# Performance work log

Hardware: AMD Instinct MI355X
Metric: run time of the kernel (lower is better)

The kernel has to match this reference:

```python
import jax, jax.numpy as jnp
import numpy as np

GROUP_SIZES = [2048, 4096, 8192, 16384]
TOP_K = 64
L1_COEFF = 1e-3
AUX_PENALTY = 1e-2
N_BATCHES_TO_DEAD = 20
AUX_K_MULT = 16


def setup_inputs() -> dict:
    D = 1024
    S = sum(GROUP_SIZES)  # 30720
    B = 2048
    key = jax.random.key(0)
    k1, k2, k3 = jax.random.split(key, 3)
    x = jax.random.normal(k1, (B, D), dtype=jnp.float32)
    # kaiming_uniform-like init for W_enc [D, S]
    bound = np.sqrt(6.0 / D)
    W_enc = jax.random.uniform(k2, (D, S), jnp.float32, -bound, bound)
    # W_dec = W_enc.T row-normalized (as in __init__)
    W_dec = W_enc.T
    W_dec = W_dec / jnp.linalg.norm(W_dec, axis=-1, keepdims=True)
    b_dec = jnp.zeros((D,), jnp.float32)
    b_enc = jnp.zeros((S,), jnp.float32)
    num_batches_not_active = jax.random.randint(k3, (S,), 0, 40, dtype=jnp.int32)
    return dict(x=x, b_dec=b_dec, b_enc=b_enc, W_enc=W_enc, W_dec=W_dec,
                num_batches_not_active=num_batches_not_active)


def reference(x, b_dec, b_enc, W_enc, W_dec, num_batches_not_active):
    B, D = x.shape
    S = W_enc.shape[1]
    # encoder
    acts = jax.nn.relu((x - b_dec) @ W_enc + b_enc)  # [B, S]
    # global (batch-level) top-k over flattened activations + scatter back
    k = TOP_K * B
    flat = acts.reshape(-1)
    vals, idx = jax.lax.top_k(flat, k)
    acts_topk = jnp.zeros_like(flat).at[idx].set(vals).reshape(B, S)
    # hierarchical group-wise decode with per-group L2 losses
    bounds = np.concatenate([[0], np.cumsum(GROUP_SIZES)]).astype(int)
    recon = jnp.broadcast_to(b_dec, (B, D))
    l2_losses = []
    for i in range(len(GROUP_SIZES)):
        s, e = int(bounds[i]), int(bounds[i + 1])
        recon = recon + acts_topk[:, s:e] @ W_dec[s:e, :]
        l2_losses.append(jnp.mean((recon - x) ** 2))
    mean_l2_loss = jnp.mean(jnp.stack(l2_losses))
    l1_loss = L1_COEFF * jnp.mean(jnp.sum(jnp.abs(acts_topk), axis=-1))
    # auxiliary dead-feature loss
    dead = num_batches_not_active >= N_BATCHES_TO_DEAD  # [S] bool
    residual = jax.lax.stop_gradient(x - recon)
    k_aux = TOP_K * AUX_K_MULT * B  # assumes num_dead * B >= k_aux (holds here)
    masked = jnp.where(dead[None, :], acts, -jnp.inf)
    min_top_k_val = jax.lax.top_k(masked.reshape(-1), k_aux)[0][-1]
    min_top_k_val = jnp.where(jnp.isfinite(min_top_k_val), min_top_k_val, 0.0)
    acts_aux = jax.nn.relu(acts - min_top_k_val) * dead[None, :].astype(acts.dtype)
    recon_aux = acts_aux @ W_dec  # dead-only contribution (others zeroed)
    aux_loss = AUX_PENALTY * jnp.mean((recon_aux - residual) ** 2)
    aux_loss = jnp.where(jnp.any(dead), aux_loss, 0.0)
    total_loss = mean_l2_loss + l1_loss + aux_loss
    l0_norm = jnp.mean(jnp.sum((acts_topk > 0).astype(jnp.float32), axis=-1))
    return total_loss, mean_l2_loss, l1_loss, aux_loss, l0_norm, acts_topk, recon
```

## Files before the change

### kernel.cpp

```cpp
#include <hip/hip_runtime.h>

#define NB 2048
#define ND 1024
#define NS 30720
#define K_MAIN 131072LL
#define K_AUX  2097152LL
#define BAND_CAP 16384
#define SEL_CAP  8192
#define CANDA_CAP 65536
#define EPS_BAND 1e-3f
#define KSPLIT 4

#define OFF_SCAL 0
#define OFF_ACC  256
#define OFF_H1M  512
#define OFF_H1A  16896
#define OFF_H2M  33280
#define OFF_H2A  49664
#define OFF_ZERO_END 66048
#define OFF_DEAD 66048
#define OFF_SEL_IDX 98304
#define OFF_SEL_BITS 131072
#define OFF_BANDI 163840
#define OFF_BANDV 229376
#define OFF_CAB  360448
#define OFF_RAUX 1048576ULL
#define OFF_AH   (OFF_RAUX + (unsigned long long)KSPLIT * NB * ND * 4)
#define OFF_AL   (OFF_AH + 2048ULL*1024*2)
#define OFF_WHT  (OFF_AL + 2048ULL*1024*2)
#define OFF_WLT  (OFF_WHT + 30720ULL*1024*2)
#define WS_NEED_ENC (OFF_WLT + 30720ULL*1024*2)
#define OFF_AXB  OFF_AH
#define OFF_WDT  (OFF_AXB + 2048ULL*30720*2)
#define WS_NEED_AUX (OFF_WDT + 1024ULL*30720*2)

#define S_NDEAD 0
#define S_B1M 1
#define S_REM1M 2
#define S_B1A 3
#define S_REM1A 4
#define S_T24M 5
#define S_BLO 6
#define S_BHI 7
#define S_T24A 8
#define S_JA 9
#define S_NHI 10
#define S_BANDC 11
#define S_CCA 12
#define S_SELCNT 13
#define S_L0 14
#define S_MINBITS 15

#define A_L2_0 0
#define A_L1 4
#define A_AUX 5

typedef __attribute__((ext_vector_type(8))) short bf16x8;
typedef __attribute__((ext_vector_type(4))) float f32x4;

__device__ __forceinline__ float blk_reduce(float v, float* sred) {
    int t = threadIdx.x;
    #pragma unroll
    for (int o = 32; o > 0; o >>= 1) v += __shfl_down(v, o, 64);
    __syncthreads();
    if ((t & 63) == 0) sred[t >> 6] = v;
    __syncthreads();
    return sred[0] + sred[1] + sred[2] + sred[3];
}

__device__ __forceinline__ unsigned short f2bf(float f) {
    unsigned u = __float_as_uint(f);
    unsigned r = (u + 0x7FFFu + ((u >> 16) & 1u)) >> 16;
    return (unsigned short)r;
}
__device__ __forceinline__ float bf2f(unsigned short h) {
    return __uint_as_float(((unsigned)h) << 16);
}

#define GLD16(gp, lp) __builtin_amdgcn_global_load_lds( \
    (const __attribute__((address_space(1))) unsigned int*)(gp), \
    (__attribute__((address_space(3))) unsigned int*)(lp), 16, 0, 0)

__global__ void k_init(int* w) {
    int n = OFF_ZERO_END / 4;
    for (int i = blockIdx.x * blockDim.x + threadIdx.x; i < n; i += gridDim.x * blockDim.x)
        w[i] = 0;
}

__global__ void k_dead(const int* __restrict__ nbna, unsigned char* __restrict__ dead, int* scal) {
    int stride = gridDim.x * blockDim.x;
    int cnt = 0;
    for (int i = blockIdx.x * blockDim.x + threadIdx.x; i < NS; i += stride) {
        bool d = nbna[i] >= 20;
        dead[i] = d ? 1 : 0;
        cnt += d ? 1 : 0;
    }
    #pragma unroll
    for (int o = 32; o > 0; o >>= 1) cnt += __shfl_down(cnt, o, 64);
    if ((threadIdx.x & 63) == 0 && cnt) atomicAdd(&scal[S_NDEAD], cnt);
}

__global__ void k_prep_a(const float* __restrict__ x, const float* __restrict__ b_dec,
                         unsigned short* __restrict__ Ahg, unsigned short* __restrict__ Alg) {
    int stride = gridDim.x * blockDim.x;
    for (int i = blockIdx.x * blockDim.x + threadIdx.x; i < NB * ND; i += stride) {
        float v = x[i] - b_dec[i & (ND - 1)];
        unsigned short h = f2bf(v);
        unsigned short l = f2bf(v - bf2f(h));
        Ahg[i] = h; Alg[i] = l;
    }
}

__global__ __launch_bounds__(256) void k_prep_w(const float* __restrict__ W,
        unsigned short* __restrict__ WhT, unsigned short* __restrict__ WlT) {
    __shared__ float tile[32][33];
    int n0 = blockIdx.x * 32, k0 = blockIdx.y * 32;
    int t = threadIdx.x;
    int c = t & 31, r = t >> 5;
    #pragma unroll
    for (int it = 0; it < 4; it++)
        tile[r + it * 8][c] = W[(size_t)(k0 + r + it * 8) * NS + n0 + c];
    __syncthreads();
    int kl = t & 31, nl = t >> 5;
    #pragma unroll
    for (int it = 0; it < 4; it++) {
        float v = tile[kl][nl + it * 8];
        unsigned short h = f2bf(v);
        unsigned short l = f2bf(v - bf2f(h));
        size_t o = (size_t)(n0 + nl + it * 8) * ND + k0 + kl;
        WhT[o] = h; WlT[o] = l;
    }
}

#define ENC_STAGE(bufoff, p, gptr, r, ktn) GLD16((gptr) + (size_t)(r) * 128 * ND + (size_t)(ktn) * 32, \
    smem + (bufoff) + (p) * 8192 + (r) * 4096 + ldsw)

#define ENC_RD_AH(boff) { _Pragma("unroll") \
    for (int i = 0; i < 8; i++) ah[i] = *(const bf16x8*)&smem[(boff) + (arb + i * 16) * 32 + cph8]; }
#define ENC_RD_BH(boff) { _Pragma("unroll") \
    for (int j = 0; j < 4; j++) bh[j] = *(const bf16x8*)&smem[(boff) + 2 * 8192 + (brb + j * 16) * 32 + cph8]; }
#define ENC_RD_BL(boff) { _Pragma("unroll") \
    for (int j = 0; j < 4; j++) bl[j] = *(const bf16x8*)&smem[(boff) + 3 * 8192 + (brb + j * 16) * 32 + cph8]; }
#define ENC_RD_AL(boff) { _Pragma("unroll") \
    for (int i = 0; i < 8; i++) al[i] = *(const bf16x8*)&smem[(boff) + 8192 + (arb + i * 16) * 32 + cph8]; }

#define ENC_MFMA(AF, BF) { \
    asm volatile("s_waitcnt lgkmcnt(0)" ::: "memory"); \
    __builtin_amdgcn_sched_barrier(0); \
    __builtin_amdgcn_s_setprio(1); \
    _Pragma("unroll") for (int i = 0; i < 8; i++) \
        _Pragma("unroll") for (int j = 0; j < 4; j++) \
            acc[i][j] = __builtin_amdgcn_mfma_f32_16x16x32_bf16(AF[i], BF[j], acc[i][j], 0, 0, 0); \
    __builtin_amdgcn_s_setprio(0); }

__global__ __launch_bounds__(512, 2) void k_enc_mfma(
        const unsigned short* __restrict__ Ahg, const unsigned short* __restrict__ Alg,
        const unsigned short* __restrict__ WhT, const unsigned short* __restrict__ WlT,
        const float* __restrict__ b_enc, float* __restrict__ acts) {
    __shared__ unsigned short smem[65536];
    const int t = threadIdx.x;
    const int lane = t & 63, w = t >> 6;
    const int wm = w >> 2, wn = w & 3;
    const int flat = blockIdx.x;
    const int wg = (flat & 7) * 120 + (flat >> 3);
    const int n0 = (wg >> 3) * 256;
    const int m0 = (wg & 7) * 256;
    const int ln15 = lane & 15, q = lane >> 4;
    const int cph8 = ((q ^ ((lane >> 1) & 3)) << 3);

    const int srow = w * 16 + (lane >> 2);
    const int sq8 = (((lane & 3) ^ ((lane >> 3) & 3)) << 3);
    const unsigned short* gA  = Ahg + (size_t)(m0 + srow) * ND + sq8;
    const unsigned short* gAl = Alg + (size_t)(m0 + srow) * ND + sq8;
    const unsigned short* gB  = WhT + (size_t)(n0 + srow) * ND + sq8;
    const unsigned short* gBl = WlT + (size_t)(n0 + srow) * ND + sq8;
    const int ldsw = w * 512;

    f32x4 acc[8][4];
    #pragma unroll
    for (int i = 0; i < 8; i++)
        #pragma unroll
        for (int j = 0; j < 4; j++) acc[i][j] = (f32x4){0.f, 0.f, 0.f, 0.f};

    const int arb = wm * 128 + ln15;
    const int brb = wn * 64 + ln15;

    ENC_STAGE(0, 0, gA, 0, 0);  ENC_STAGE(0, 0, gA, 1, 0);
    ENC_STAGE(0, 2, gB, 0, 0);  ENC_STAGE(0, 2, gB, 1, 0);
    ENC_STAGE(0, 3, gBl, 0, 0); ENC_STAGE(0, 3, gBl, 1, 0);
    ENC_STAGE(0, 1, gAl, 0, 0); ENC_STAGE(0, 1, gAl, 1, 0);

    for (int kt = 0; kt < 31; ++kt) {
        const int cboff = (kt & 1) * 32768;
        const int nboff = cboff ^ 32768;
        const int kn = kt + 1;
        bf16x8 ah[8], bh[4], bl[4], al[8];

        ENC_STAGE(nboff, 0, gA, 0, kn);  ENC_STAGE(nboff, 0, gA, 1, kn);
        ENC_STAGE(nboff, 2, gB, 0, kn);  ENC_STAGE(nboff, 2, gB, 1, kn);
        asm volatile("s_waitcnt vmcnt(8)" ::: "memory");
        __builtin_amdgcn_s_barrier();
        ENC_RD_AH(cboff) ENC_RD_BH(cboff)
        ENC_MFMA(ah, bh)

        ENC_STAGE(nboff, 3, gBl, 0, kn); ENC_STAGE(nboff, 3, gBl, 1, kn);
        ENC_STAGE(nboff, 1, gAl, 0, kn); ENC_STAGE(nboff, 1, gAl, 1, kn);
        asm volatile("s_waitcnt vmcnt(8)" ::: "memory");
        __builtin_amdgcn_s_barrier();
        ENC_RD_BL(cboff)
        ENC_MFMA(ah, bl)

        ENC_RD_AL(cboff)
        ENC_MFMA(al, bh)
    }

    {
        const int cboff = 32768;
        bf16x8 ah[8], bh[4], bl[4], al[8];
        asm volatile("s_waitcnt vmcnt(4)" ::: "memory");
        __builtin_amdgcn_s_barrier();
        ENC_RD_AH(cboff) ENC_RD_BH(cboff)
        ENC_MFMA(ah, bh)
        asm volatile("s_waitcnt vmcnt(0)" ::: "memory");
        __builtin_amdgcn_s_barrier();
        ENC_RD_BL(cboff)
        ENC_MFMA(ah, bl)
        ENC_RD_AL(cboff)
        ENC_MFMA(al, bh)
    }

    #pragma unroll
    for (int j = 0; j < 4; j++) {
        int n = n0 + wn * 64 + j * 16 + ln15;
        float be = b_enc[n];
        #pragma unroll
        for (int i = 0; i < 8; i++) {
            int mrow = m0 + wm * 128 + i * 16 + q * 4;
            #pragma unroll
            for (int rg = 0; rg < 4; rg++)
                acts[(size_t)(mrow + rg) * NS + n] = fmaxf(acc[i][j][rg] + be, 0.f);
        }
    }
}

#define GBM 128
#define GBN 128
#define GBK 8
__global__ __launch_bounds__(256) void k_enc_gemm(const float* __restrict__ x,
        const float* __restrict__ b_dec, const float* __restrict__ b_enc,
        const float* __restrict__ W, float* __restrict__ acts) {
    __shared__ float As[GBK][GBM];
    __shared__ float Bs[GBK][GBN];
    const int t = threadIdx.x;
    const int tx = t & 15, ty = t >> 4;
    const int m0 = blockIdx.y * GBM, n0 = blockIdx.x * GBN;
    const int am = t >> 1, ak = (t & 1) * 4;
    const int bk = t >> 5, bnq = (t & 31) * 4;
    float acc[8][8];
    #pragma unroll
    for (int i = 0; i < 8; i++)
        #pragma unroll
        for (int j = 0; j < 8; j++) acc[i][j] = 0.f;
    for (int k0 = 0; k0 < ND; k0 += GBK) {
        float4 av = *(const float4*)(x + (size_t)(m0 + am) * ND + k0 + ak);
        float4 bd = *(const float4*)(b_dec + k0 + ak);
        As[ak + 0][am] = av.x - bd.x;
        As[ak + 1][am] = av.y - bd.y;
        As[ak + 2][am] = av.z - bd.z;
        As[ak + 3][am] = av.w - bd.w;
        *(float4*)&Bs[bk][bnq] = *(const float4*)(W + (size_t)(k0 + bk) * NS + n0 + bnq);
        __syncthreads();
        #pragma unroll
        for (int kk = 0; kk < GBK; kk++) {
            float a[8], b[8];
            *(float4*)&a[0] = *(const float4*)&As[kk][ty * 4];
            *(float4*)&a[4] = *(const float4*)&As[kk][64 + ty * 4];
            *(float4*)&b[0] = *(const float4*)&Bs[kk][tx * 4];
            *(float4*)&b[4] = *(const float4*)&Bs[kk][64 + tx * 4];
            #pragma unroll
            for (int i = 0; i < 8; i++)
                #pragma unroll
                for (int j = 0; j < 8; j++)
                    acc[i][j] = fmaf(a[i], b[j], acc[i][j]);
        }
        __syncthreads();
    }
    float be[8];
    #pragma unroll
    for (int j = 0; j < 4; j++) {
        be[j]     = b_enc[n0 + tx * 4 + j];
        be[4 + j] = b_enc[n0 + 64 + tx * 4 + j];
    }
    #pragma unroll
    for (int i = 0; i < 8; i++) {
        int row = m0 + ((i < 4) ? (ty * 4 + i) : (64 + ty * 4 + i - 4));
        float* orow = acts + (size_t)row * NS + n0;
        #pragma unroll
        for (int j = 0; j < 4; j++) {
            orow[tx * 4 + j]      = fmaxf(acc[i][j] + be[j], 0.f);
            orow[64 + tx * 4 + j] = fmaxf(acc[i][4 + j] + be[4 + j], 0.f);
        }
    }
}

__global__ __launch_bounds__(256) void k_hist1(const float* __restrict__ acts,
        const unsigned char* __restrict__ dead, int* h1m, int* h1a) {
    __shared__ int hm[4096], ha[4096];
    int t = threadIdx.x;
    for (int i = t; i < 4096; i += 256) { hm[i] = 0; ha[i] = 0; }
    __syncthreads();
    for (int row = blockIdx.x; row < NB; row += gridDim.x) {
        const float* pr = acts + (size_t)row * NS;
        for (int c = t; c < NS; c += 256) {
            unsigned bits = __float_as_uint(pr[c]);
            bool isz = (bits == 0u);
            bool dd = dead[c] != 0;
            unsigned long long mz = __ballot(isz);
            unsigned long long mza = __ballot(isz && dd);
            if ((t & 63) == 0) {
                int nz = __popcll(mz);
                if (nz) atomicAdd(&hm[0], nz);
                int nza = __popcll(mza);
                if (nza) atomicAdd(&ha[0], nza);
            }
            if (!isz) {
                atomicAdd(&hm[bits >> 20], 1);
                if (dd) atomicAdd(&ha[bits >> 20], 1);
            }
        }
    }
    __syncthreads();
    for (int i = t; i < 4096; i += 256) {
        if (hm[i]) atomicAdd(&h1m[i], hm[i]);
        if (ha[i]) atomicAdd(&h1a[i], ha[i]);
    }
}

__global__ void k_scan(const int* __restrict__ hist, int* scal, int mode) {
    __shared__ long long csum[256];
    __shared__ long long totsh;
    int t = threadIdx.x;
    int base = t * 16;
    int h[16];
    long long loc = 0;
    #pragma unroll
    for (int i = 0; i < 16; i++) { h[i] = hist[base + i]; loc += h[i]; }
    csum[t] = loc;
    __syncthreads();
    if (t == 0) {
        long long run = 0;
        for (int c = 255; c >= 0; c--) { long long tmp = csum[c]; csum[c] = run; run += tmp; }
        totsh = run;
    }
    __syncthreads();
    long long k;
    if (mode == 0) k = K_MAIN;
    else if (mode == 1) k = K_AUX;
    else if (mode == 2) k = (long long)scal[S_REM1M];
    else {
        if (scal[S_B1A] < 0) { if (t == 0) { scal[S_T24A] = -1; scal[S_MINBITS] = 0; } return; }
        k = (long long)scal[S_REM1A];
    }
    if (mode == 1 && k > totsh) { if (t == 0) scal[S_B1A] = -1; return; }
    long long cum = csum[t];
    int fb = -1; long long rem = 0;
    for (int i = 15; i >= 0; i--) {
        long long ca = cum;
        cum += h[i];
        if (ca < k && k <= cum) { fb = base + i; rem = k - ca; }
    }
    if (fb >= 0) {
        if (mode == 0)      { scal[S_B1M] = fb; scal[S_REM1M] = (int)rem; }
        else if (mode == 1) { scal[S_B1A] = fb; scal[S_REM1A] = (int)rem; }
        else if (mode == 2) {
            int t24 = (scal[S_B1M] << 12) | fb;
            scal[S_T24M] = t24;
            float center = __uint_as_float((((unsigned)t24) << 8) | 128u);
            float lo = center - EPS_BAND;
            if (lo < 0.f) lo = 0.f;
            scal[S_BLO] = (int)__float_as_uint(lo);
            scal[S_BHI] = (int)__float_as_uint(center + EPS_BAND);
        }
        else { scal[S_T24A] = (scal[S_B1A] << 12) | fb; scal[S_JA] = (int)rem; }
    }
}

__global__ __launch_bounds__(256) void k_hist2(const float* __restrict__ acts,
        const unsigned char* __restrict__ dead, const int* scal, int* h2m, int* h2a) {
    int b1m = scal[S_B1M], b1a = scal[S_B1A];
    int row = blockIdx.x, t = threadIdx.x;
    const float* pr = acts + (size_t)row * NS;
    for (int c = t; c < NS; c += 256) {
        unsigned bits = __float_as_uint(pr[c]);
        int hi = (int)(bits >> 20);
        if (hi == b1m) atomicAdd(&h2m[(bits >> 8) & 0xFFF], 1);
        if (b1a >= 0 && hi == b1a && dead[c]) atomicAdd(&h2a[(bits >> 8) & 0xFFF], 1);
    }
}

__global__ __launch_bounds__(256) void k_collect(const float* __restrict__ acts,
        const unsigned char* __restrict__ dead, int* scal,
        int* bandi, unsigned* cab) {
    int row = blockIdx.x, t = threadIdx.x;
    unsigned blo = (unsigned)scal[S_BLO], bhi = (unsigned)scal[S_BHI];
    int t24a = scal[S_T24A];
    const float* pr = acts + (size_t)row * NS;
    int cnt = 0;
    for (int c = t; c < NS; c += 256) {
        unsigned bits = __float_as_uint(pr[c]);
        if (bits > bhi) cnt++;
        else if (bits >= blo) {
            int p = atomicAdd(&scal[S_BANDC], 1);
            if (p < BAND_CAP) bandi[p] = row * NS + c;
        }
        if (t24a >= 0 && (bits >> 8) == (unsigned)t24a && dead[c]) {
            int p = atomicAdd(&scal[S_CCA], 1);
            if (p < CANDA_CAP) cab[p] = bits;
        }
    }
    #pragma unroll
    for (int o = 32; o > 0; o >>= 1) cnt += __shfl_down(cnt, o, 64);
    __shared__ int s2[4];
    if ((t & 63) == 0) s2[t >> 6] = cnt;
    __syncthreads();
    if (t == 0) {
        int tot = s2[0] + s2[1] + s2[2] + s2[3];
        if (tot) atomicAdd(&scal[S_NHI], tot);
    }
}

__global__ __launch_bounds__(256) void k_resolve(const unsigned* __restrict__ cab, int* scal) {
    __shared__ int h[256];
    int t = threadIdx.x;
    h[t] = 0;
    __syncthreads();
    int t24a = scal[S_T24A];
    if (t24a < 0) { if (t == 0) scal[S_MINBITS] = 0; return; }
    int cnt = min(scal[S_CCA], CANDA_CAP);
    int ja = scal[S_JA];
    for (int e = t; e < cnt; e += 256) atomicAdd(&h[cab[e] & 0xFF], 1);
    __syncthreads();
    if (t == 0) {
        long long cum = 0; int L = 0;
        for (int b = 255; b >= 0; b--) {
            long long ca = cum; cum += h[b];
            if (ca < ja && ja <= cum) { L = b; break; }
        }
        scal[S_MINBITS] = (int)((((unsigned)t24a) << 8) | (unsigned)L);
    }
}

__global__ __launch_bounds__(256) void k_band_re(const float* __restrict__ x,
        const float* __restrict__ b_dec, const float* __restrict__ b_enc,
        const float* __restrict__ W, const int* scal,
        const int* __restrict__ bandi, double* __restrict__ bandv) {
    int n = min(scal[S_BANDC], BAND_CAP);
    int t = threadIdx.x;
    __shared__ double sd[4];
    for (int e = blockIdx.x; e < n; e += gridDim.x) {
        int idx = bandi[e];
        int r = idx / NS, c = idx - r * NS;
        double s = 0.0;
        #pragma unroll
        for (int j = 0; j < 4; j++) {
            int d = t + j * 256;
            s += ((double)x[(size_t)r * ND + d] - (double)b_dec[d]) * (double)W[(size_t)d * NS + c];
        }
        #pragma unroll
        for (int o = 32; o > 0; o >>= 1) s += __shfl_down(s, o, 64);
        if ((t & 63) == 0) sd[t >> 6] = s;
        __syncthreads();
        if (t == 0) {
            double v = sd[0] + sd[1] + sd[2] + sd[3] + (double)b_enc[c];
            bandv[e] = fmax(v, 0.0);
        }
        __syncthreads();
    }
}

__global__ __launch_bounds__(256) void k_band_sel(int* scal,
        const int* __restrict__ bandi, const double* __restrict__ bandv,
        int* sel_idx, unsigned* sel_bits) {
    int n = min(scal[S_BANDC], BAND_CAP);
    int need = (int)(K_MAIN - (long long)scal[S_NHI]);
    if (need < 0) need = 0;
    if (need > n) need = n;
    int t = threadIdx.x;
    for (int e = t; e < n; e += 256) {
        double v = bandv[e];
        int idx = bandi[e];
        int rank = 0;
        for (int j = 0; j < n; j++) {
            double vj = bandv[j];
            rank += (vj > v || (vj == v && bandi[j] < idx)) ? 1 : 0;
        }
        if (rank < need) {
            int p = atomicAdd(&scal[S_SELCNT], 1);
            if (p < SEL_CAP) { sel_idx[p] = idx; sel_bits[p] = __float_as_uint((float)v); }
        }
    }
}

__global__ __launch_bounds__(256) void k_decode(const float* __restrict__ acts,
        const float* __restrict__ x, const float* __restrict__ b_dec, const float* __restrict__ Wd,
        float* __restrict__ recon, const int* scal,
        const int* __restrict__ sel_idx, double* acc) {
    int row = blockIdx.x, t = threadIdx.x;
    unsigned blo = (unsigned)scal[S_BLO], bhi = (unsigned)scal[S_BHI];
    int selcnt = min(scal[S_SELCNT], SEL_CAP);
    __shared__ int lj[2048];
    __shared__ float lv[2048];
    __shared__ int lcnt;
    __shared__ float sred[4];
    const int d0 = t * 4;
    float4 r;
    r.x = b_dec[d0]; r.y = b_dec[d0 + 1]; r.z = b_dec[d0 + 2]; r.w = b_dec[d0 + 3];
    float4 xv = *(const float4*)(x + (size_t)row * ND + d0);
    const float* arow = acts + (size_t)row * NS;
    const int bnds[5] = {0, 2048, 6144, 14336, NS};
    for (int g = 0; g < 4; g++) {
        for (int c0 = bnds[g]; c0 < bnds[g + 1]; c0 += 2048) {
            __syncthreads();
            if (t == 0) lcnt = 0;
            __syncthreads();
            #pragma unroll
            for (int u = 0; u < 8; u++) {
                int c = c0 + u * 256 + t;
                float v = arow[c];
                unsigned bits = __float_as_uint(v);
                bool keep = bits > bhi;
                if (!keep && bits >= blo) {
                    int flat = row * NS + c;
                    for (int e = 0; e < selcnt; e++)
                        if (sel_idx[e] == flat) { keep = true; break; }
                }
                if (keep) { int p = atomicAdd(&lcnt, 1); lj[p] = c; lv[p] = v; }
            }
            __syncthreads();
            int n = lcnt;
            for (int e = 0; e < n; e++) {
                float a_ = lv[e];
                float4 w = *(const float4*)(Wd + (size_t)lj[e] * ND + d0);
                r.x = fmaf(a_, w.x, r.x);
                r.y = fmaf(a_, w.y, r.y);
                r.z = fmaf(a_, w.z, r.z);
                r.w = fmaf(a_, w.w, r.w);
            }
        }
        float dx = r.x - xv.x, dy = r.y - xv.y, dz = r.z - xv.z, dw = r.w - xv.w;
        float ss = dx * dx + dy * dy + dz * dz + dw * dw;
        float tot = blk_reduce(ss, sred);
        if (t == 0) atomicAdd(&acc[A_L2_0 + g], (double)tot);
    }
    float* orow = recon + (size_t)row * ND + d0;
    orow[0] = r.x; orow[1] = r.y; orow[2] = r.z; orow[3] = r.w;
}

__global__ __launch_bounds__(256) void k_aux_pack(const float* __restrict__ acts,
        const unsigned char* __restrict__ dead, const int* scal,
        unsigned short* __restrict__ axb) {
    int row = blockIdx.x, t = threadIdx.x;
    float minval = __uint_as_float((unsigned)scal[S_MINBITS]);
    const float* arow = acts + (size_t)row * NS;
    unsigned short* orow = axb + (size_t)row * NS;
    for (int c = t; c < NS; c += 256) {
        float v = arow[c];
        float o = (dead[c] && v > minval) ? (v - minval) : 0.f;
        orow[c] = f2bf(o);
    }
}

__global__ __launch_bounds__(256) void k_prep_wd(const float* __restrict__ Wd,
        unsigned short* __restrict__ WdT) {
    __shared__ float tile[32][33];
    int s0 = blockIdx.x * 32, d0 = blockIdx.y * 32;
    int t = threadIdx.x;
    int c = t & 31, r = t >> 5;
    #pragma unroll
    for (int it = 0; it < 4; it++)
        tile[r + it * 8][c] = Wd[(size_t)(s0 + r + it * 8) * ND + d0 + c];
    __syncthreads();
    int sl = t & 31, dl = t >> 5;
    #pragma unroll
    for (int it = 0; it < 4; it++)
        WdT[(size_t)(d0 + dl + it * 8) * NS + s0 + sl] = f2bf(tile[sl][dl + it * 8]);
}

__global__ __launch_bounds__(256) void k_aux_mfma(
        const unsigned short* __restrict__ axb, const unsigned short* __restrict__ WdT,
        float* __restrict__ raux) {
    __shared__ unsigned short As[128 * 32], Bs[128 * 32];
    const int t = threadIdx.x;
    const int lane = t & 63, w = t >> 6;
    const int wm = w >> 1, wn = w & 1;
    const int m0 = blockIdx.y * 128, n0 = blockIdx.x * 128;
    const int kbase = blockIdx.z * (NS / KSPLIT);
    const int ln15 = lane & 15, q = lane >> 4;

    f32x4 acc[4][4];
    #pragma unroll
    for (int i = 0; i < 4; i++)
        #pragma unroll
        for (int j = 0; j < 4; j++) acc[i][j] = (f32x4){0.f, 0.f, 0.f, 0.f};

    const unsigned short* gbase;
    unsigned short* lbase;
    if (w < 2) { gbase = axb + (size_t)(m0 + w * 64) * NS; lbase = As + w * 64 * 32; }
    else       { gbase = WdT + (size_t)(n0 + (w - 2) * 64) * NS; lbase = Bs + (w - 2) * 64 * 32; }
    const unsigned short* glane = gbase + (size_t)(lane >> 2) * NS + (lane & 3) * 8 + kbase;

    for (int k0 = 0; k0 < NS / KSPLIT; k0 += 32) {
        __syncthreads();
        #pragma unroll
        for (int ch = 0; ch < 4; ch++)
            GLD16(glane + (size_t)ch * 16 * NS + k0, lbase + ch * 512);
        __syncthreads();

        bf16x8 af[4];
        #pragma unroll
        for (int i = 0; i < 4; i++)
            af[i] = *(const bf16x8*)&As[(wm * 64 + i * 16 + ln15) * 32 + q * 8];
        #pragma unroll
        for (int j = 0; j < 4; j++) {
            bf16x8 bf = *(const bf16x8*)&Bs[(wn * 64 + j * 16 + ln15) * 32 + q * 8];
            #pragma unroll
            for (int i = 0; i < 4; i++)
                acc[i][j] = __builtin_amdgcn_mfma_f32_16x16x32_bf16(af[i], bf, acc[i][j], 0, 0, 0);
        }
    }
    float* rz = raux + (size_t)blockIdx.z * NB * ND;
    #pragma unroll
    for (int j = 0; j < 4; j++) {
        int n = n0 + wn * 64 + j * 16 + ln15;
        #pragma unroll
        for (int i = 0; i < 4; i++) {
            int mrow = m0 + wm * 64 + i * 16 + q * 4;
            #pragma unroll
            for (int rg = 0; rg < 4; rg++)
                rz[(size_t)(mrow + rg) * ND + n] = acc[i][j][rg];
        }
    }
}

__global__ __launch_bounds__(256) void k_aux_diff(const float* __restrict__ raux,
        const float* __restrict__ x, const float* __restrict__ recon, double* acc) {
    __shared__ float sred[4];
    float ss = 0.f;
    int stride = gridDim.x * blockDim.x;
    for (int i = blockIdx.x * blockDim.x + threadIdx.x; i < NB * ND; i += stride) {
        float ra = raux[i];
        #pragma unroll
        for (int z = 1; z < KSPLIT; z++) ra += raux[(size_t)z * NB * ND + i];
        float d = ra - (x[i] - recon[i]);
        ss += d * d;
    }
    float tot = blk_reduce(ss, sred);
    if (threadIdx.x == 0) atomicAdd(&acc[A_AUX], (double)tot);
}

__global__ __launch_bounds__(256) void k_aux(const float* __restrict__ acts,
        const unsigned char* __restrict__ dead, const float* __restrict__ x,
        const float* __restrict__ recon, const float* __restrict__ Wd,
        const int* scal, double* acc) {
    int row = blockIdx.x, t = threadIdx.x;
    float minval = __uint_as_float((unsigned)scal[S_MINBITS]);
    __shared__ int lj[2048];
    __shared__ float lv[2048];
    __shared__ int lcnt;
    __shared__ float sred[4];
    float4 r = {0.f, 0.f, 0.f, 0.f};
    const float* arow = acts + (size_t)row * NS;
    const int d0 = t * 4;
    for (int c0 = 0; c0 < NS; c0 += 2048) {
        __syncthreads();
        if (t == 0) lcnt = 0;
        __syncthreads();
        #pragma unroll
        for (int u = 0; u < 8; u++) {
            int c = c0 + u * 256 + t;
            float v = arow[c];
            if (dead[c] && v > minval) {
                int p = atomicAdd(&lcnt, 1);
                lj[p] = c; lv[p] = v - minval;
            }
        }
        __syncthreads();
        int n = lcnt;
        for (int e = 0; e < n; e++) {
            float a_ = lv[e];
            float4 w = *(const float4*)(Wd + (size_t)lj[e] * ND + d0);
            r.x = fmaf(a_, w.x, r.x);
            r.y = fmaf(a_, w.y, r.y);
            r.z = fmaf(a_, w.z, r.z);
            r.w = fmaf(a_, w.w, r.w);
        }
    }
    const float* xr = x + (size_t)row * ND + d0;
    const float* rr = recon + (size_t)row * ND + d0;
    float dx = r.x - (xr[0] - rr[0]);
    float dy = r.y - (xr[1] - rr[1]);
    float dz = r.z - (xr[2] - rr[2]);
    float dw = r.w - (xr[3] - rr[3]);
    float ss = dx * dx + dy * dy + dz * dz + dw * dw;
    float tot = blk_reduce(ss, sred);
    if (t == 0) atomicAdd(&acc[A_AUX], (double)tot);
}

__global__ __launch_bounds__(256) void k_topk_write(float* __restrict__ out, const int* scal, double* acc, int* scalw) {
    unsigned bhi = (unsigned)scal[S_BHI];
    float l1 = 0.f;
    int cnt = 0;
    const long long vstart = 8, nvec = 15728639;
    long long stride = (long long)gridDim.x * blockDim.x;
    for (long long i = (long long)blockIdx.x * blockDim.x + threadIdx.x; i < nvec; i += stride) {
        float4* p = (float4*)(out + vstart) + i;
        float4 v = *p;
        #define PROC(F) { unsigned b = __float_as_uint(v.F); if (b > bhi) { l1 += v.F; cnt++; } else v.F = 0.f; }
        PROC(x) PROC(y) PROC(z) PROC(w)
        #undef PROC
        *p = v;
    }
    if (blockIdx.x == 0 && threadIdx.x == 0) {
        const long long head[4] = {5, 6, 7, 62914564LL};
        for (int q = 0; q < 4; q++) {
            float v = out[head[q]];
            unsigned b = __float_as_uint(v);
            if (b > bhi) { l1 += v; cnt++; } else out[head[q]] = 0.f;
        }
    }
    int t = threadIdx.x;
    #pragma unroll
    for (int o = 32; o > 0; o >>= 1) { l1 += __shfl_down(l1, o, 64); cnt += __shfl_down(cnt, o, 64); }
    __shared__ float s1[4];
    __shared__ int s2[4];
    if ((t & 63) == 0) { s1[t >> 6] = l1; s2[t >> 6] = cnt; }
    __syncthreads();
    if (t == 0) {
        atomicAdd(&acc[A_L1], (double)(s1[0] + s1[1] + s1[2] + s1[3]));
        atomicAdd(&scalw[S_L0], s2[0] + s2[1] + s2[2] + s2[3]);
    }
}

__global__ __launch_bounds__(256) void k_selwrite(float* __restrict__ acts, const int* __restrict__ sel_idx,
        const unsigned* __restrict__ sel_bits, int* scal, double* acc) {
    int t = threadIdx.x;
    int n = min(scal[S_SELCNT], SEL_CAP);
    float l1 = 0.f;
    for (int e = t; e < n; e += 256) {
        float v = __uint_as_float(sel_bits[e]);
        acts[sel_idx[e]] = v;
        l1 += v;
    }
    #pragma unroll
    for (int o = 32; o > 0; o >>= 1) l1 += __shfl_down(l1, o, 64);
    __shared__ float s1[4];
    if ((t & 63) == 0) s1[t >> 6] = l1;
    __syncthreads();
    if (t == 0) {
        atomicAdd(&acc[A_L1], (double)(s1[0] + s1[1] + s1[2] + s1[3]));
        atomicAdd(&scal[S_L0], n);
    }
}

__global__ void k_final(float* out, const int* scal, const double* acc) {
    if (threadIdx.x == 0 && blockIdx.x == 0) {
        double ml2 = (acc[0] + acc[1] + acc[2] + acc[3]) * 0.25 / ((double)NB * ND);
        double l1 = 1e-3 * acc[A_L1] / (double)NB;
        double aux = (scal[S_NDEAD] > 0) ? (1e-2 * acc[A_AUX] / ((double)NB * ND)) : 0.0;
        out[0] = (float)(ml2 + l1 + aux);
        out[1] = (float)ml2;
        out[2] = (float)l1;
        out[3] = (float)aux;
        out[4] = (float)scal[S_L0] / (float)NB;
    }
}

extern "C" void kernel_launch(void* const* d_in, const int* in_sizes, int n_in,
                              void* d_out, int out_size, void* d_ws, size_t ws_size,
                              hipStream_t stream) {
    const float* x     = (const float*)d_in[0];
    const float* b_dec = (const float*)d_in[1];
    const float* b_enc = (const float*)d_in[2];
    const float* W_enc = (const float*)d_in[3];
    const float* W_dec = (const float*)d_in[4];
    const int*   nbna  = (const int*)d_in[5];

    float* out = (float*)d_out;
    float* acts  = out + 5;
    float* recon = out + 5 + (size_t)NB * NS;

    char* ws = (char*)d_ws;
    int*    scal = (int*)(ws + OFF_SCAL);
    double* acc  = (double*)(ws + OFF_ACC);
    int*    h1m  = (int*)(ws + OFF_H1M);
    int*    h1a  = (int*)(ws + OFF_H1A);
    int*    h2m  = (int*)(ws + OFF_H2M);
    int*    h2a  = (int*)(ws + OFF_H2A);
    unsigned char* dead = (unsigned char*)(ws + OFF_DEAD);
    int*      sel_idx  = (int*)(ws + OFF_SEL_IDX);
    unsigned* sel_bits = (unsigned*)(ws + OFF_SEL_BITS);
    int*      bandi = (int*)(ws + OFF_BANDI);
    double*   bandv = (double*)(ws + OFF_BANDV);
    unsigned* cab   = (unsigned*)(ws + OFF_CAB);
    float*    raux  = (float*)(ws + OFF_RAUX);
    unsigned short* Ahg = (unsigned short*)(ws + OFF_AH);
    unsigned short* Alg = (unsigned short*)(ws + OFF_AL);
    unsigned short* WhT = (unsigned short*)(ws + OFF_WHT);
    unsigned short* WlT = (unsigned short*)(ws + OFF_WLT);
    unsigned short* axb = (unsigned short*)(ws + OFF_AXB);
    unsigned short* WdT = (unsigned short*)(ws + OFF_WDT);

    const bool use_mfma     = (ws_size >= WS_NEED_ENC);
    const bool use_aux_gemm = (ws_size >= WS_NEED_AUX);

    k_init<<<64, 256, 0, stream>>>((int*)d_ws);
    k_dead<<<60, 256, 0, stream>>>(nbna, dead, scal);
    if (use_mfma) {
        k_prep_a<<<512, 256, 0, stream>>>(x, b_dec, Ahg, Alg);
        k_prep_w<<<dim3(NS / 32, ND / 32), 256, 0, stream>>>(W_enc, WhT, WlT);
        k_enc_mfma<<<(NB / 256) * (NS / 256), 512, 0, stream>>>(Ahg, Alg, WhT, WlT, b_enc, acts);
    } else {
        k_enc_gemm<<<dim3(NS / GBN, NB / GBM), 256, 0, stream>>>(x, b_dec, b_enc, W_enc, acts);
    }
    k_hist1<<<1024, 256, 0, stream>>>(acts, dead, h1m, h1a);
    k_scan<<<1, 256, 0, stream>>>(h1m, scal, 0);
    k_scan<<<1, 256, 0, stream>>>(h1a, scal, 1);
    k_hist2<<<NB, 256, 0, stream>>>(acts, dead, scal, h2m, h2a);
    k_scan<<<1, 256, 0, stream>>>(h2m, scal, 2);
    k_scan<<<1, 256, 0, stream>>>(h2a, scal, 3);
    k_collect<<<NB, 256, 0, stream>>>(acts, dead, scal, bandi, cab);
    k_resolve<<<1, 256, 0, stream>>>(cab, scal);
    k_band_re<<<512, 256, 0, stream>>>(x, b_dec, b_enc, W_enc, scal, bandi, bandv);
    k_band_sel<<<1, 256, 0, stream>>>(scal, bandi, bandv, sel_idx, sel_bits);
    k_decode<<<NB, 256, 0, stream>>>(acts, x, b_dec, W_dec, recon, scal, sel_idx, acc);
    if (use_aux_gemm) {
        k_aux_pack<<<NB, 256, 0, stream>>>(acts, dead, scal, axb);
        k_prep_wd<<<dim3(NS / 32, ND / 32), 256, 0, stream>>>(W_dec, WdT);
        k_aux_mfma<<<dim3(ND / 128, NB / 128, KSPLIT), 256, 0, stream>>>(axb, WdT, raux);
        k_aux_diff<<<512, 256, 0, stream>>>(raux, x, recon, acc);
    } else {
        k_aux<<<NB, 256, 0, stream>>>(acts, dead, x, recon, W_dec, scal, acc);
    }
    k_topk_write<<<4096, 256, 0, stream>>>(out, scal, acc, scal);
    k_selwrite<<<1, 256, 0, stream>>>(acts, sel_idx, sel_bits, scal, acc);
    k_final<<<1, 64, 0, stream>>>(out, scal, acc);
}
```

Before: 2.029 ms.

## Shrink encoder MFMA tile to 256x128 with single-barrier double-buffered pipeline

Changes the split-bf16 encoder GEMM tile from 256x256 to 256x128. The warp grid goes from 2x4 to 4x2, with 4x4 accumulators per warp, and the grid doubles to 1920 blocks. The main loop now issues all next-tile loads after one barrier per k-step and staggers LDS reads with partial lgkmcnt waits so MFMA bursts can start early. LDS drops to 96KB per block and per-thread register use falls. In exchange, arithmetic intensity per block is lower and more global traffic goes to the B operand.

```diff
diff --git a/kernel.cpp b/kernel.cpp
--- a/kernel.cpp
+++ b/kernel.cpp
@@ -132,23 +132,29 @@
     }
 }
 
-#define ENC_STAGE(bufoff, p, gptr, r, ktn) GLD16((gptr) + (size_t)(r) * 128 * ND + (size_t)(ktn) * 32, \
-    smem + (bufoff) + (p) * 8192 + (r) * 4096 + ldsw)
+#define ENC_BUF 24576
+#define ENC_PAH 0
+#define ENC_PAL 8192
+#define ENC_PBH 16384
+#define ENC_PBL 20480
+
+#define ENC_STAGE_A(boff, plane, gptr, r, ktn) GLD16((gptr) + (size_t)(r) * 128 * ND + (size_t)(ktn) * 32, \
+    smem + (boff) + (plane) + (r) * 4096 + ldsw)
+#define ENC_STAGE_B(boff, plane, gptr, ktn) GLD16((gptr) + (size_t)(ktn) * 32, \
+    smem + (boff) + (plane) + ldsw)
 
 #define ENC_RD_AH(boff) { _Pragma("unroll") \
-    for (int i = 0; i < 8; i++) ah[i] = *(const bf16x8*)&smem[(boff) + (arb + i * 16) * 32 + cph8]; }
+    for (int i = 0; i < 4; i++) ah[i] = *(const bf16x8*)&smem[(boff) + ENC_PAH + (arb + i * 16) * 32 + cph8]; }
+#define ENC_RD_AL(boff) { _Pragma("unroll") \
+    for (int i = 0; i < 4; i++) al[i] = *(const bf16x8*)&smem[(boff) + ENC_PAL + (arb + i * 16) * 32 + cph8]; }
 #define ENC_RD_BH(boff) { _Pragma("unroll") \
-    for (int j = 0; j < 4; j++) bh[j] = *(const bf16x8*)&smem[(boff) + 2 * 8192 + (brb + j * 16) * 32 + cph8]; }
+    for (int j = 0; j < 4; j++) bh[j] = *(const bf16x8*)&smem[(boff) + ENC_PBH + (brb + j * 16) * 32 + cph8]; }
 #define ENC_RD_BL(boff) { _Pragma("unroll") \
-    for (int j = 0; j < 4; j++) bl[j] = *(const bf16x8*)&smem[(boff) + 3 * 8192 + (brb + j * 16) * 32 + cph8]; }
-#define ENC_RD_AL(boff) { _Pragma("unroll") \
-    for (int i = 0; i < 8; i++) al[i] = *(const bf16x8*)&smem[(boff) + 8192 + (arb + i * 16) * 32 + cph8]; }
-
-#define ENC_MFMA(AF, BF) { \
-    asm volatile("s_waitcnt lgkmcnt(0)" ::: "memory"); \
-    __builtin_amdgcn_sched_barrier(0); \
+    for (int j = 0; j < 4; j++) bl[j] = *(const bf16x8*)&smem[(boff) + ENC_PBL + (brb + j * 16) * 32 + cph8]; }
+
+#define ENC_MFMA_BURST(AF, BF) { \
     __builtin_amdgcn_s_setprio(1); \
-    _Pragma("unroll") for (int i = 0; i < 8; i++) \
+    _Pragma("unroll") for (int i = 0; i < 4; i++) \
         _Pragma("unroll") for (int j = 0; j < 4; j++) \
             acc[i][j] = __builtin_amdgcn_mfma_f32_16x16x32_bf16(AF[i], BF[j], acc[i][j], 0, 0, 0); \
     __builtin_amdgcn_s_setprio(0); }
@@ -157,13 +163,13 @@
         const unsigned short* __restrict__ Ahg, const unsigned short* __restrict__ Alg,
         const unsigned short* __restrict__ WhT, const unsigned short* __restrict__ WlT,
         const float* __restrict__ b_enc, float* __restrict__ acts) {
-    __shared__ unsigned short smem[65536];
+    __shared__ unsigned short smem[49152];
     const int t = threadIdx.x;
     const int lane = t & 63, w = t >> 6;
-    const int wm = w >> 2, wn = w & 3;
+    const int wm = w >> 1, wn = w & 1;
     const int flat = blockIdx.x;
-    const int wg = (flat & 7) * 120 + (flat >> 3);
-    const int n0 = (wg >> 3) * 256;
+    const int wg = (flat & 7) * 240 + (flat >> 3);
+    const int n0 = (wg >> 3) * 128;
     const int m0 = (wg & 7) * 256;
     const int ln15 = lane & 15, q = lane >> 4;
     const int cph8 = ((q ^ ((lane >> 1) & 3)) << 3);
@@ -176,57 +182,47 @@
     const unsigned short* gBl = WlT + (size_t)(n0 + srow) * ND + sq8;
     const int ldsw = w * 512;
 
-    f32x4 acc[8][4];
-    #pragma unroll
-    for (int i = 0; i < 8; i++)
+    f32x4 acc[4][4];
+    #pragma unroll
+    for (int i = 0; i < 4; i++)
         #pragma unroll
         for (int j = 0; j < 4; j++) acc[i][j] = (f32x4){0.f, 0.f, 0.f, 0.f};
 
-    const int arb = wm * 128 + ln15;
+    const int arb = wm * 64 + ln15;
     const int brb = wn * 64 + ln15;
 
-    ENC_STAGE(0, 0, gA, 0, 0);  ENC_STAGE(0, 0, gA, 1, 0);
-    ENC_STAGE(0, 2, gB, 0, 0);  ENC_STAGE(0, 2, gB, 1, 0);
-    ENC_STAGE(0, 3, gBl, 0, 0); ENC_STAGE(0, 3, gBl, 1, 0);
-    ENC_STAGE(0, 1, gAl, 0, 0); ENC_STAGE(0, 1, gAl, 1, 0);
-
-    for (int kt = 0; kt < 31; ++kt) {
-        const int cboff = (kt & 1) * 32768;
-        const int nboff = cboff ^ 32768;
-        const int kn = kt + 1;
-        bf16x8 ah[8], bh[4], bl[4], al[8];
-
-        ENC_STAGE(nboff, 0, gA, 0, kn);  ENC_STAGE(nboff, 0, gA, 1, kn);
-        ENC_STAGE(nboff, 2, gB, 0, kn);  ENC_STAGE(nboff, 2, gB, 1, kn);
-        asm volatile("s_waitcnt vmcnt(8)" ::: "memory");
-        __builtin_amdgcn_s_barrier();
-        ENC_RD_AH(cboff) ENC_RD_BH(cboff)
-        ENC_MFMA(ah, bh)
-
-        ENC_STAGE(nboff, 3, gBl, 0, kn); ENC_STAGE(nboff, 3, gBl, 1, kn);
-        ENC_STAGE(nboff, 1, gAl, 0, kn); ENC_STAGE(nboff, 1, gAl, 1, kn);
-        asm volatile("s_waitcnt vmcnt(8)" ::: "memory");
-        __builtin_amdgcn_s_barrier();
-        ENC_RD_BL(cboff)
-        ENC_MFMA(ah, bl)
-
-        ENC_RD_AL(cboff)
-        ENC_MFMA(al, bh)
-    }
-
-    {
-        const int cboff = 32768;
-        bf16x8 ah[8], bh[4], bl[4], al[8];
-        asm volatile("s_waitcnt vmcnt(4)" ::: "memory");
-        __builtin_amdgcn_s_barrier();
-        ENC_RD_AH(cboff) ENC_RD_BH(cboff)
-        ENC_MFMA(ah, bh)
+    ENC_STAGE_A(0, ENC_PAH, gA, 0, 0);  ENC_STAGE_A(0, ENC_PAH, gA, 1, 0);
+    ENC_STAGE_A(0, ENC_PAL, gAl, 0, 0); ENC_STAGE_A(0, ENC_PAL, gAl, 1, 0);
+    ENC_STAGE_B(0, ENC_PBH, gB, 0);     ENC_STAGE_B(0, ENC_PBL, gBl, 0);
+
+    for (int kt = 0; kt < 32; ++kt) {
+        const int cboff = (kt & 1) * ENC_BUF;
+        const int nboff = cboff ^ ENC_BUF;
+        bf16x8 ah[4], bh[4], bl[4], al[4];
+
         asm volatile("s_waitcnt vmcnt(0)" ::: "memory");
         __builtin_amdgcn_s_barrier();
+        __builtin_amdgcn_sched_barrier(0);
+        if (kt < 31) {
+            const int kn = kt + 1;
+            ENC_STAGE_A(nboff, ENC_PAH, gA, 0, kn);  ENC_STAGE_A(nboff, ENC_PAH, gA, 1, kn);
+            ENC_STAGE_A(nboff, ENC_PAL, gAl, 0, kn); ENC_STAGE_A(nboff, ENC_PAL, gAl, 1, kn);
+            ENC_STAGE_B(nboff, ENC_PBH, gB, kn);     ENC_STAGE_B(nboff, ENC_PBL, gBl, kn);
+        }
+
+        ENC_RD_AH(cboff) ENC_RD_BH(cboff)
+        __builtin_amdgcn_sched_barrier(0);
         ENC_RD_BL(cboff)
-        ENC_MFMA(ah, bl)
+        asm volatile("s_waitcnt lgkmcnt(4)" ::: "memory");
+        __builtin_amdgcn_sched_barrier(0);
+        ENC_MFMA_BURST(ah, bh)
         ENC_RD_AL(cboff)
-        ENC_MFMA(al, bh)
+        asm volatile("s_waitcnt lgkmcnt(4)" ::: "memory");
+        __builtin_amdgcn_sched_barrier(0);
+        ENC_MFMA_BURST(ah, bl)
+        asm volatile("s_waitcnt lgkmcnt(0)" ::: "memory");
+        __builtin_amdgcn_sched_barrier(0);
+        ENC_MFMA_BURST(al, bh)
     }
 
     #pragma unroll
@@ -234,8 +230,8 @@
         int n = n0 + wn * 64 + j * 16 + ln15;
         float be = b_enc[n];
         #pragma unroll
-        for (int i = 0; i < 8; i++) {
-            int mrow = m0 + wm * 128 + i * 16 + q * 4;
+        for (int i = 0; i < 4; i++) {
+            int mrow = m0 + wm * 64 + i * 16 + q * 4;
             #pragma unroll
             for (int rg = 0; rg < 4; rg++)
                 acts[(size_t)(mrow + rg) * NS + n] = fmaxf(acc[i][j][rg] + be, 0.f);
@@ -818,7 +814,7 @@
     if (use_mfma) {
         k_prep_a<<<512, 256, 0, stream>>>(x, b_dec, Ahg, Alg);
         k_prep_w<<<dim3(NS / 32, ND / 32), 256, 0, stream>>>(W_enc, WhT, WlT);
-        k_enc_mfma<<<(NB / 256) * (NS / 256), 512, 0, stream>>>(Ahg, Alg, WhT, WlT, b_enc, acts);
+        k_enc_mfma<<<(NB / 256) * (NS / 128), 512, 0, stream>>>(Ahg, Alg, WhT, WlT, b_enc, acts);
     } else {
         k_enc_gemm<<<dim3(NS / GBN, NB / GBM), 256, 0, stream>>>(x, b_dec, b_enc, W_enc, acts);
     }
```

Result: slower. 2.105 ms (+3.8%).

## Restructure encoder MFMA loop with single barrier and overlapped LDS reads

Applied to the files above, without the earlier changes.

The encoder GEMM main loop now issues all eight next-tile global-to-LDS stages at once after one vmcnt(0) wait and one barrier per k-step, instead of two half-batches each with its own barrier. LDS fragment reads for the B-low and A-low operands are prefetched while earlier MFMA bursts run, using partial lgkmcnt waits instead of a full drain before each burst. The peeled final iteration is folded into the loop. This cuts barriers per iteration and hides LDS latency behind MFMAs, but waiting for all global loads before each step may expose more global-memory latency.

```diff
diff --git a/kernel.cpp b/kernel.cpp
--- a/kernel.cpp
+++ b/kernel.cpp
@@ -137,16 +137,14 @@
 
 #define ENC_RD_AH(boff) { _Pragma("unroll") \
     for (int i = 0; i < 8; i++) ah[i] = *(const bf16x8*)&smem[(boff) + (arb + i * 16) * 32 + cph8]; }
+#define ENC_RD_AL(boff) { _Pragma("unroll") \
+    for (int i = 0; i < 8; i++) al[i] = *(const bf16x8*)&smem[(boff) + 8192 + (arb + i * 16) * 32 + cph8]; }
 #define ENC_RD_BH(boff) { _Pragma("unroll") \
     for (int j = 0; j < 4; j++) bh[j] = *(const bf16x8*)&smem[(boff) + 2 * 8192 + (brb + j * 16) * 32 + cph8]; }
 #define ENC_RD_BL(boff) { _Pragma("unroll") \
     for (int j = 0; j < 4; j++) bl[j] = *(const bf16x8*)&smem[(boff) + 3 * 8192 + (brb + j * 16) * 32 + cph8]; }
-#define ENC_RD_AL(boff) { _Pragma("unroll") \
-    for (int i = 0; i < 8; i++) al[i] = *(const bf16x8*)&smem[(boff) + 8192 + (arb + i * 16) * 32 + cph8]; }
-
-#define ENC_MFMA(AF, BF) { \
-    asm volatile("s_waitcnt lgkmcnt(0)" ::: "memory"); \
-    __builtin_amdgcn_sched_barrier(0); \
+
+#define ENC_MFMA_BURST(AF, BF) { \
     __builtin_amdgcn_s_setprio(1); \
     _Pragma("unroll") for (int i = 0; i < 8; i++) \
         _Pragma("unroll") for (int j = 0; j < 4; j++) \
@@ -190,43 +188,35 @@
     ENC_STAGE(0, 3, gBl, 0, 0); ENC_STAGE(0, 3, gBl, 1, 0);
     ENC_STAGE(0, 1, gAl, 0, 0); ENC_STAGE(0, 1, gAl, 1, 0);
 
-    for (int kt = 0; kt < 31; ++kt) {
+    for (int kt = 0; kt < 32; ++kt) {
         const int cboff = (kt & 1) * 32768;
         const int nboff = cboff ^ 32768;
-        const int kn = kt + 1;
         bf16x8 ah[8], bh[4], bl[4], al[8];
 
-        ENC_STAGE(nboff, 0, gA, 0, kn);  ENC_STAGE(nboff, 0, gA, 1, kn);
-        ENC_STAGE(nboff, 2, gB, 0, kn);  ENC_STAGE(nboff, 2, gB, 1, kn);
-        asm volatile("s_waitcnt vmcnt(8)" ::: "memory");
-        __builtin_amdgcn_s_barrier();
-        ENC_RD_AH(cboff) ENC_RD_BH(cboff)
-        ENC_MFMA(ah, bh)
-
-        ENC_STAGE(nboff, 3, gBl, 0, kn); ENC_STAGE(nboff, 3, gBl, 1, kn);
-        ENC_STAGE(nboff, 1, gAl, 0, kn); ENC_STAGE(nboff, 1, gAl, 1, kn);
-        asm volatile("s_waitcnt vmcnt(8)" ::: "memory");
-        __builtin_amdgcn_s_barrier();
-        ENC_RD_BL(cboff)
-        ENC_MFMA(ah, bl)
-
-        ENC_RD_AL(cboff)
-        ENC_MFMA(al, bh)
-    }
-
-    {
-        const int cboff = 32768;
-        bf16x8 ah[8], bh[4], bl[4], al[8];
-        asm volatile("s_waitcnt vmcnt(4)" ::: "memory");
-        __builtin_amdgcn_s_barrier();
-        ENC_RD_AH(cboff) ENC_RD_BH(cboff)
-        ENC_MFMA(ah, bh)
         asm volatile("s_waitcnt vmcnt(0)" ::: "memory");
         __builtin_amdgcn_s_barrier();
+        __builtin_amdgcn_sched_barrier(0);
+        if (kt < 31) {
+            const int kn = kt + 1;
+            ENC_STAGE(nboff, 0, gA, 0, kn);  ENC_STAGE(nboff, 0, gA, 1, kn);
+            ENC_STAGE(nboff, 2, gB, 0, kn);  ENC_STAGE(nboff, 2, gB, 1, kn);
+            ENC_STAGE(nboff, 3, gBl, 0, kn); ENC_STAGE(nboff, 3, gBl, 1, kn);
+            ENC_STAGE(nboff, 1, gAl, 0, kn); ENC_STAGE(nboff, 1, gAl, 1, kn);
+        }
+
+        ENC_RD_AH(cboff) ENC_RD_BH(cboff)
+        __builtin_amdgcn_sched_barrier(0);
         ENC_RD_BL(cboff)
-        ENC_MFMA(ah, bl)
+        asm volatile("s_waitcnt lgkmcnt(4)" ::: "memory");
+        __builtin_amdgcn_sched_barrier(0);
+        ENC_MFMA_BURST(ah, bh)
         ENC_RD_AL(cboff)
-        ENC_MFMA(al, bh)
+        asm volatile("s_waitcnt lgkmcnt(8)" ::: "memory");
+        __builtin_amdgcn_sched_barrier(0);
+        ENC_MFMA_BURST(ah, bl)
+        asm volatile("s_waitcnt lgkmcnt(0)" ::: "memory");
+        __builtin_amdgcn_sched_barrier(0);
+        ENC_MFMA_BURST(al, bh)
     }
 
     #pragma unroll
```

Measured after the change: 2.070 ms. 2.0% more time.

## Fuse histogram into encoder epilogue and fuse aux pack/topk write into decode

Applied to the files above, without the earlier changes.

The first-level histogram is now built in the MFMA encoder epilogue with shared-memory atomics, which removes a separate full pass over the activation matrix. The decode kernel now also zeroes non-selected activations in place, packs the aux bf16 input and accumulates L1 and L0 counts. That removes the separate k_aux_pack and k_topk_write passes over acts. The cost is LDS atomic contention in the encoder epilogue and extra global writes in decode. There is also a possible ordering dependency, since acts are overwritten before k_selwrite reads them.

```diff
diff --git a/kernel.cpp b/kernel.cpp
--- a/kernel.cpp
+++ b/kernel.cpp
@@ -137,12 +137,12 @@
 
 #define ENC_RD_AH(boff) { _Pragma("unroll") \
     for (int i = 0; i < 8; i++) ah[i] = *(const bf16x8*)&smem[(boff) + (arb + i * 16) * 32 + cph8]; }
+#define ENC_RD_AL(boff) { _Pragma("unroll") \
+    for (int i = 0; i < 8; i++) al[i] = *(const bf16x8*)&smem[(boff) + 8192 + (arb + i * 16) * 32 + cph8]; }
 #define ENC_RD_BH(boff) { _Pragma("unroll") \
     for (int j = 0; j < 4; j++) bh[j] = *(const bf16x8*)&smem[(boff) + 2 * 8192 + (brb + j * 16) * 32 + cph8]; }
 #define ENC_RD_BL(boff) { _Pragma("unroll") \
     for (int j = 0; j < 4; j++) bl[j] = *(const bf16x8*)&smem[(boff) + 3 * 8192 + (brb + j * 16) * 32 + cph8]; }
-#define ENC_RD_AL(boff) { _Pragma("unroll") \
-    for (int i = 0; i < 8; i++) al[i] = *(const bf16x8*)&smem[(boff) + 8192 + (arb + i * 16) * 32 + cph8]; }
 
 #define ENC_MFMA(AF, BF) { \
     asm volatile("s_waitcnt lgkmcnt(0)" ::: "memory"); \
@@ -156,7 +156,8 @@
 __global__ __launch_bounds__(512, 2) void k_enc_mfma(
         const unsigned short* __restrict__ Ahg, const unsigned short* __restrict__ Alg,
         const unsigned short* __restrict__ WhT, const unsigned short* __restrict__ WlT,
-        const float* __restrict__ b_enc, float* __restrict__ acts) {
+        const float* __restrict__ b_enc, const unsigned char* __restrict__ dead,
+        float* __restrict__ acts, int* __restrict__ h1m, int* __restrict__ h1a) {
     __shared__ unsigned short smem[65536];
     const int t = threadIdx.x;
     const int lane = t & 63, w = t >> 6;
@@ -229,17 +230,41 @@
         ENC_MFMA(al, bh)
     }
 
+    __syncthreads();
+    int* hm = (int*)smem;
+    int* ha = hm + 4096;
+    for (int i2 = t; i2 < 8192; i2 += 512) hm[i2] = 0;
+    __syncthreads();
+
+    int zc = 0, zca = 0;
     #pragma unroll
     for (int j = 0; j < 4; j++) {
         int n = n0 + wn * 64 + j * 16 + ln15;
         float be = b_enc[n];
+        bool dd = dead[n] != 0;
         #pragma unroll
         for (int i = 0; i < 8; i++) {
             int mrow = m0 + wm * 128 + i * 16 + q * 4;
             #pragma unroll
-            for (int rg = 0; rg < 4; rg++)
-                acts[(size_t)(mrow + rg) * NS + n] = fmaxf(acc[i][j][rg] + be, 0.f);
-        }
+            for (int rg = 0; rg < 4; rg++) {
+                float v = fmaxf(acc[i][j][rg] + be, 0.f);
+                acts[(size_t)(mrow + rg) * NS + n] = v;
+                unsigned bits = __float_as_uint(v);
+                if (bits == 0u) { zc++; zca += dd ? 1 : 0; }
+                else {
+                    atomicAdd(&hm[bits >> 20], 1);
+                    if (dd) atomicAdd(&ha[bits >> 20], 1);
+                }
+            }
+        }
+    }
+    #pragma unroll
+    for (int o = 32; o > 0; o >>= 1) { zc += __shfl_down(zc, o, 64); zca += __shfl_down(zca, o, 64); }
+    if ((t & 63) == 0) { if (zc) atomicAdd(&hm[0], zc); if (zca) atomicAdd(&ha[0], zca); }
+    __syncthreads();
+    for (int i2 = t; i2 < 4096; i2 += 512) {
+        if (hm[i2]) atomicAdd(&h1m[i2], hm[i2]);
+        if (ha[i2]) atomicAdd(&h1a[i2], ha[i2]);
     }
 }
 
@@ -501,12 +526,14 @@
     }
 }
 
-__global__ __launch_bounds__(256) void k_decode(const float* __restrict__ acts,
+__global__ __launch_bounds__(256) void k_decode(float* __restrict__ acts,
         const float* __restrict__ x, const float* __restrict__ b_dec, const float* __restrict__ Wd,
-        float* __restrict__ recon, const int* scal,
-        const int* __restrict__ sel_idx, double* acc) {
+        float* __restrict__ recon, const unsigned char* __restrict__ dead,
+        const int* __restrict__ sel_idx, unsigned short* __restrict__ axb,
+        int* scal, double* acc, int fuse) {
     int row = blockIdx.x, t = threadIdx.x;
     unsigned blo = (unsigned)scal[S_BLO], bhi = (unsigned)scal[S_BHI];
+    float minval = __uint_as_float((unsigned)scal[S_MINBITS]);
     int selcnt = min(scal[S_SELCNT], SEL_CAP);
     __shared__ int lj[2048];
     __shared__ float lv[2048];
@@ -516,7 +543,9 @@
     float4 r;
     r.x = b_dec[d0]; r.y = b_dec[d0 + 1]; r.z = b_dec[d0 + 2]; r.w = b_dec[d0 + 3];
     float4 xv = *(const float4*)(x + (size_t)row * ND + d0);
-    const float* arow = acts + (size_t)row * NS;
+    float* arow = acts + (size_t)row * NS;
+    unsigned short* xrow = axb + (size_t)row * NS;
+    float l1 = 0.f; int kcnt = 0;
     const int bnds[5] = {0, 2048, 6144, 14336, NS};
     for (int g = 0; g < 4; g++) {
         for (int c0 = bnds[g]; c0 < bnds[g + 1]; c0 += 2048) {
@@ -528,13 +557,20 @@
                 int c = c0 + u * 256 + t;
                 float v = arow[c];
                 unsigned bits = __float_as_uint(v);
-                bool keep = bits > bhi;
+                bool strict = bits > bhi;
+                bool keep = strict;
                 if (!keep && bits >= blo) {
                     int flat = row * NS + c;
                     for (int e = 0; e < selcnt; e++)
                         if (sel_idx[e] == flat) { keep = true; break; }
                 }
                 if (keep) { int p = atomicAdd(&lcnt, 1); lj[p] = c; lv[p] = v; }
+                if (fuse) {
+                    if (strict) { l1 += v; kcnt++; }
+                    arow[c] = strict ? v : 0.f;
+                    float o = (dead[c] && v > minval) ? (v - minval) : 0.f;
+                    xrow[c] = f2bf(o);
+                }
             }
             __syncthreads();
             int n = lcnt;
@@ -554,6 +590,18 @@
     }
     float* orow = recon + (size_t)row * ND + d0;
     orow[0] = r.x; orow[1] = r.y; orow[2] = r.z; orow[3] = r.w;
+    if (fuse) {
+        #pragma unroll
+        for (int o = 32; o > 0; o >>= 1) { l1 += __shfl_down(l1, o, 64); kcnt += __shfl_down(kcnt, o, 64); }
+        __shared__ float s1[4];
+        __shared__ int s2[4];
+        if ((t & 63) == 0) { s1[t >> 6] = l1; s2[t >> 6] = kcnt; }
+        __syncthreads();
+        if (t == 0) {
+            atomicAdd(&acc[A_L1], (double)(s1[0] + s1[1] + s1[2] + s1[3]));
+            atomicAdd(&scal[S_L0], s2[0] + s2[1] + s2[2] + s2[3]);
+        }
+    }
 }
 
 __global__ __launch_bounds__(256) void k_aux_pack(const float* __restrict__ acts,
@@ -818,11 +866,11 @@
     if (use_mfma) {
         k_prep_a<<<512, 256, 0, stream>>>(x, b_dec, Ahg, Alg);
         k_prep_w<<<dim3(NS / 32, ND / 32), 256, 0, stream>>>(W_enc, WhT, WlT);
-        k_enc_mfma<<<(NB / 256) * (NS / 256), 512, 0, stream>>>(Ahg, Alg, WhT, WlT, b_enc, acts);
+        k_enc_mfma<<<(NB / 256) * (NS / 256), 512, 0, stream>>>(Ahg, Alg, WhT, WlT, b_enc, dead, acts, h1m, h1a);
     } else {
         k_enc_gemm<<<dim3(NS / GBN, NB / GBM), 256, 0, stream>>>(x, b_dec, b_enc, W_enc, acts);
-    }
-    k_hist1<<<1024, 256, 0, stream>>>(acts, dead, h1m, h1a);
+        k_hist1<<<1024, 256, 0, stream>>>(acts, dead, h1m, h1a);
+    }
     k_scan<<<1, 256, 0, stream>>>(h1m, scal, 0);
     k_scan<<<1, 256, 0, stream>>>(h1a, scal, 1);
     k_hist2<<<NB, 256, 0, stream>>>(acts, dead, scal, h2m, h2a);
@@ -832,16 +880,16 @@
     k_resolve<<<1, 256, 0, stream>>>(cab, scal);
     k_band_re<<<512, 256, 0, stream>>>(x, b_dec, b_enc, W_enc, scal, bandi, bandv);
     k_band_sel<<<1, 256, 0, stream>>>(scal, bandi, bandv, sel_idx, sel_bits);
-    k_decode<<<NB, 256, 0, stream>>>(acts, x, b_dec, W_dec, recon, scal, sel_idx, acc);
     if (use_aux_gemm) {
-        k_aux_pack<<<NB, 256, 0, stream>>>(acts, dead, scal, axb);
+        k_decode<<<NB, 256, 0, stream>>>(acts, x, b_dec, W_dec, recon, dead, sel_idx, axb, scal, acc, 1);
         k_prep_wd<<<dim3(NS / 32, ND / 32), 256, 0, stream>>>(W_dec, WdT);
         k_aux_mfma<<<dim3(ND / 128, NB / 128, KSPLIT), 256, 0, stream>>>(axb, WdT, raux);
         k_aux_diff<<<512, 256, 0, stream>>>(raux, x, recon, acc);
     } else {
+        k_decode<<<NB, 256, 0, stream>>>(acts, x, b_dec, W_dec, recon, dead, sel_idx, axb, scal, acc, 0);
         k_aux<<<NB, 256, 0, stream>>>(acts, dead, x, recon, W_dec, scal, acc);
-    }
-    k_topk_write<<<4096, 256, 0, stream>>>(out, scal, acc, scal);
+        k_topk_write<<<4096, 256, 0, stream>>>(out, scal, acc, scal);
+    }
     k_selwrite<<<1, 256, 0, stream>>>(acts, sel_idx, sel_bits, scal, acc);
     k_final<<<1, 64, 0, stream>>>(out, scal, acc);
 }
```

Measured after the change: 1.901 ms. -6.3%, faster.
